# Optimization experiments

Hardware: AMD Instinct MI355X
Metric: run time of the kernel (lower is better)

The kernel has to match this reference:

```python
import jax, jax.numpy as jnp
import numpy as np

N = 100000
E = 3200000
D_IN = 512
D_HID = 128
D_OUT = 4


def setup_inputs() -> dict:
    key = jax.random.key(0)
    k1, k2, k3, k4, k5, k6 = jax.random.split(key, 6)
    x = jax.random.normal(k1, (N, D_IN), dtype=jnp.float32)
    edge_index = jax.random.randint(k2, (2, E), 0, N, dtype=jnp.int64)
    # GCNConv params (Glorot-ish scale)
    W1 = jax.random.normal(k3, (D_IN, D_HID), dtype=jnp.float32) / np.sqrt(D_IN)
    b1 = jax.random.normal(k4, (D_HID,), dtype=jnp.float32) * 0.01
    W2 = jax.random.normal(k5, (D_HID, D_OUT), dtype=jnp.float32) / np.sqrt(D_HID)
    b2 = jax.random.normal(k6, (D_OUT,), dtype=jnp.float32) * 0.01
    return {"x": x, "edge_index": edge_index, "W1": W1, "b1": b1, "W2": W2, "b2": b2}


def _gcn_conv(x, W, b, src, dst, deg_inv_sqrt):
    # h = X W, then symmetric-normalized aggregation with self-loops (PyG GCNConv default)
    h = x @ W                                   # [N, F_out]
    norm = deg_inv_sqrt[src] * deg_inv_sqrt[dst]  # [E]
    agg = jax.ops.segment_sum(h[src] * norm[:, None], dst, num_segments=x.shape[0])
    # self-loop contribution: norm_ii = deg_inv_sqrt[i]^2
    agg = agg + h * (deg_inv_sqrt ** 2)[:, None]
    return agg + b


def reference(x, edge_index, W1, b1, W2, b2):
    src, dst = edge_index[0], edge_index[1]
    # degree with added self-loops (edge weights = 1)
    deg = jax.ops.segment_sum(jnp.ones((E,), dtype=x.dtype), dst, num_segments=N) + 1.0
    deg_inv_sqrt = jax.lax.rsqrt(deg)
    h = jax.nn.relu(_gcn_conv(x, W1, b1, src, dst, deg_inv_sqrt))
    out = _gcn_conv(h, W2, b2, src, dst, deg_inv_sqrt)
    return out
```

## Files before the change

kernel.cpp:

```cpp
#include <hip/hip_runtime.h>
#include <hip/hip_fp16.h>

#define DIN 512
#define DHID 128
#define DOUT 4
#define BSH 8
#define PA_CHUNK 8192

typedef _Float16 f16x8 __attribute__((ext_vector_type(8)));
typedef _Float16 f16x4 __attribute__((ext_vector_type(4)));
typedef float    f32x4 __attribute__((ext_vector_type(4)));

#define GLOAD_LDS(gp, lp)                                                     \
  __builtin_amdgcn_global_load_lds(                                           \
      (const __attribute__((address_space(1))) void*)(gp),                    \
      (__attribute__((address_space(3))) void*)(lp), 16, 0, 0)

__global__ void detect_i64_k(const int* __restrict__ raw, int* __restrict__ flag) {
  if (blockIdx.x == 0 && threadIdx.x == 0) {
    int z = 1;
    for (int k = 0; k < 8; ++k)
      if (raw[2 * k + 1] != 0) z = 0;
    flag[0] = z;
  }
}

__global__ __launch_bounds__(256) void bcount_k(const int* __restrict__ raw,
                                                const int* __restrict__ flag,
                                                int* __restrict__ gbcnt, int E) {
  __shared__ int h[512];
  const int tid = threadIdx.x;
  const int f = flag[0];
  for (int i = tid; i < 512; i += 256) h[i] = 0;
  __syncthreads();
  const size_t e0 = (size_t)blockIdx.x * PA_CHUNK;
  #pragma unroll
  for (int k = 0; k < 32; ++k) {
    size_t e = e0 + (size_t)k * 256 + tid;
    if (e < (size_t)E) {
      int d = f ? raw[2 * ((size_t)E + e)] : raw[(size_t)E + e];
      atomicAdd(&h[d >> BSH], 1);
    }
  }
  __syncthreads();
  for (int i = tid; i < 512; i += 256)
    if (h[i]) atomicAdd(&gbcnt[i], h[i]);
}

__global__ __launch_bounds__(512) void bscan_k(const int* __restrict__ gbcnt,
                                               int* __restrict__ boffs,
                                               int* __restrict__ bcur,
                                               int* __restrict__ offs,
                                               int nbkt, int N, int E) {
  __shared__ int sm[512];
  int t = threadIdx.x;
  int v = (t < nbkt) ? gbcnt[t] : 0;
  int x = v;
  sm[t] = x;
  __syncthreads();
  #pragma unroll
  for (int o = 1; o < 512; o <<= 1) {
    int y = (t >= o) ? sm[t - o] : 0;
    __syncthreads();
    x += y;
    sm[t] = x;
    __syncthreads();
  }
  if (t < nbkt) {
    boffs[t] = x - v;
    bcur[t] = x - v;
  }
  if (t == 0) {
    boffs[nbkt] = E;
    offs[N] = E;
  }
}

__global__ __launch_bounds__(256) void binA_k(const int* __restrict__ raw,
                                              const int* __restrict__ flag,
                                              int* __restrict__ bcur,
                                              unsigned* __restrict__ pairs, int E) {
  __shared__ int hist[512];
  __shared__ int base[512];
  const int tid = threadIdx.x;
  const int f = flag[0];
  const size_t e0 = (size_t)blockIdx.x * PA_CHUNK;
  for (int i = tid; i < 512; i += 256) hist[i] = 0;
  __syncthreads();
  int es[32], ed[32];
  #pragma unroll
  for (int k = 0; k < 32; ++k) {
    size_t e = e0 + (size_t)k * 256 + tid;
    if (e < (size_t)E) {
      es[k] = f ? raw[2 * e] : raw[e];
      ed[k] = f ? raw[2 * ((size_t)E + e)] : raw[(size_t)E + e];
      atomicAdd(&hist[ed[k] >> BSH], 1);
    } else {
      ed[k] = -1;
    }
  }
  __syncthreads();
  for (int i = tid; i < 512; i += 256) {
    int c = hist[i];
    base[i] = c ? atomicAdd(&bcur[i], c) : 0;
    hist[i] = 0;
  }
  __syncthreads();
  #pragma unroll
  for (int k = 0; k < 32; ++k) {
    if (ed[k] >= 0) {
      int b = ed[k] >> BSH;
      int pos = base[b] + atomicAdd(&hist[b], 1);
      pairs[pos] = ((unsigned)es[k] << 8) | ((unsigned)ed[k] & 255u);
    }
  }
}

__global__ __launch_bounds__(256) void binB_k(const unsigned* __restrict__ pairs,
                                              const int* __restrict__ boffs,
                                              int* __restrict__ csr,
                                              int* __restrict__ offs,
                                              float* __restrict__ dis, int N) {
  __shared__ int lcnt[256];
  __shared__ int sc[256];
  const int tid = threadIdx.x;
  const int n0 = blockIdx.x << BSH;
  const int lo = boffs[blockIdx.x];
  const int hi = boffs[blockIdx.x + 1];
  lcnt[tid] = 0;
  __syncthreads();
  for (int j = lo + tid; j < hi; j += 256) atomicAdd(&lcnt[(int)(pairs[j] & 255u)], 1);
  __syncthreads();
  int v = lcnt[tid];
  int x = v;
  sc[tid] = x;
  __syncthreads();
  #pragma unroll
  for (int o = 1; o < 256; o <<= 1) {
    int y = (tid >= o) ? sc[tid - o] : 0;
    __syncthreads();
    x += y;
    sc[tid] = x;
    __syncthreads();
  }
  const int base = lo + x - v;
  const int node = n0 + tid;
  if (node < N) {
    offs[node] = base;
    dis[node] = rsqrtf((float)v + 1.0f);
  }
  __syncthreads();
  lcnt[tid] = base;
  __syncthreads();
  for (int j = lo + tid; j < hi; j += 256) {
    unsigned p = pairs[j];
    int dl = (int)(p & 255u);
    int pos = atomicAdd(&lcnt[dl], 1);
    csr[pos] = (int)(p >> 8);
  }
}

__global__ __launch_bounds__(256) void wsplit_k(const float* __restrict__ W1,
                                                __half* __restrict__ Bt2) {
  int idx = blockIdx.x * 256 + threadIdx.x;
  if (idx >= DIN * DHID) return;
  int k = idx >> 7;
  int n = idx & 127;
  int kt = k >> 5, kk = k & 31;
  float w = W1[idx];
  _Float16 hi = (_Float16)w;
  _Float16 lo = (_Float16)(w - (float)hi);
  size_t base = (size_t)(kt * 128 + n) * 64;
  Bt2[base + kk]      = *(__half*)&hi;
  Bt2[base + 32 + kk] = *(__half*)&lo;
}

__global__ __launch_bounds__(256, 2) void gemm1_k(const float* __restrict__ A,
                                                  const __half* __restrict__ Bt2,
                                                  const float* __restrict__ dis,
                                                  __half* __restrict__ hs, int N) {
  __shared__ char smem[49152];
  char* const sB = smem + 32768;
  const int tid = threadIdx.x;
  const int wave = tid >> 6, lane = tid & 63;
  const int lr = lane & 15, quad = lane >> 4;
  const int m0 = blockIdx.x * 128;
  const int mbase = (wave >> 1) * 64;
  const int nbase = (wave & 1) * 64;
  const int wbase = (tid & ~63) * 16;

  f32x4 acc[4][4];
  #pragma unroll
  for (int mt = 0; mt < 4; ++mt)
    #pragma unroll
    for (int nt = 0; nt < 4; ++nt) acc[mt][nt] = (f32x4){0.f, 0.f, 0.f, 0.f};

  const float*  agp[4];
  const __half* bgp[4];
  #pragma unroll
  for (int l = 0; l < 4; ++l) {
    int d16 = l * 256 + tid;
    int row = d16 >> 3;
    int chk = (d16 & 7) ^ (row & 7);
    int gr = m0 + row;
    if (gr >= N) gr = N - 1;
    agp[l] = A + (size_t)gr * DIN + chk * 4;
    bgp[l] = Bt2 + (size_t)row * 64 + chk * 8;
  }

  #pragma unroll
  for (int l = 0; l < 4; ++l)
    GLOAD_LDS(agp[l], smem + l * 4096 + wbase);
  #pragma unroll
  for (int l = 0; l < 4; ++l)
    GLOAD_LDS(bgp[l], sB + l * 4096 + wbase);

  int cur = 0;
  for (int kt = 0; kt < 16; ++kt) {
    if (kt < 15) {
      char* dA = smem + (cur ^ 1) * 16384;
      #pragma unroll
      for (int l = 0; l < 4; ++l)
        GLOAD_LDS(agp[l] + (kt + 1) * 32, dA + l * 4096 + wbase);
      asm volatile("s_waitcnt vmcnt(4)" ::: "memory");
    } else {
      asm volatile("s_waitcnt vmcnt(0)" ::: "memory");
    }
    __builtin_amdgcn_s_barrier();
    asm volatile("" ::: "memory");
    char* sA = smem + cur * 16384;
    f16x8 ah[4], al[4];
    #pragma unroll
    for (int mt = 0; mt < 4; ++mt) {
      int r = mbase + mt * 16 + lr;
      f32x4 v0 = *(const f32x4*)(sA + r * 128 + (((2 * quad + 0) ^ (r & 7)) << 4));
      f32x4 v1 = *(const f32x4*)(sA + r * 128 + (((2 * quad + 1) ^ (r & 7)) << 4));
      _Float16 c0 = (_Float16)v0[0], c1 = (_Float16)v0[1],
               c2 = (_Float16)v0[2], c3 = (_Float16)v0[3],
               c4 = (_Float16)v1[0], c5 = (_Float16)v1[1],
               c6 = (_Float16)v1[2], c7 = (_Float16)v1[3];
      ah[mt] = (f16x8){c0, c1, c2, c3, c4, c5, c6, c7};
      al[mt] = (f16x8){(_Float16)(v0[0] - (float)c0), (_Float16)(v0[1] - (float)c1),
                       (_Float16)(v0[2] - (float)c2), (_Float16)(v0[3] - (float)c3),
                       (_Float16)(v1[0] - (float)c4), (_Float16)(v1[1] - (float)c5),
                       (_Float16)(v1[2] - (float)c6), (_Float16)(v1[3] - (float)c7)};
    }
    #pragma unroll
    for (int nt = 0; nt < 4; ++nt) {
      int c = nbase + nt * 16 + lr;
      f16x8 bh = *(const f16x8*)(sB + c * 128 + (((0 + quad) ^ (c & 7)) << 4));
      f16x8 bl = *(const f16x8*)(sB + c * 128 + (((4 + quad) ^ (c & 7)) << 4));
      #pragma unroll
      for (int mt = 0; mt < 4; ++mt)
        acc[mt][nt] = __builtin_amdgcn_mfma_f32_16x16x32_f16(al[mt], bh, acc[mt][nt], 0, 0, 0);
      #pragma unroll
      for (int mt = 0; mt < 4; ++mt)
        acc[mt][nt] = __builtin_amdgcn_mfma_f32_16x16x32_f16(ah[mt], bl, acc[mt][nt], 0, 0, 0);
      #pragma unroll
      for (int mt = 0; mt < 4; ++mt)
        acc[mt][nt] = __builtin_amdgcn_mfma_f32_16x16x32_f16(ah[mt], bh, acc[mt][nt], 0, 0, 0);
    }
    __builtin_amdgcn_sched_barrier(0);
    __builtin_amdgcn_s_barrier();
    asm volatile("" ::: "memory");
    if (kt < 15) {
      #pragma unroll
      for (int l = 0; l < 4; ++l)
        GLOAD_LDS(bgp[l] + (size_t)(kt + 1) * 8192, sB + l * 4096 + wbase);
    }
    cur ^= 1;
  }
  _Float16* sep = (_Float16*)smem;
  #pragma unroll
  for (int mt = 0; mt < 4; ++mt) {
    #pragma unroll
    for (int r = 0; r < 4; ++r) {
      int row = mbase + mt * 16 + quad * 4 + r;
      int gr = m0 + row;
      float dv = dis[gr < N ? gr : (N - 1)];
      #pragma unroll
      for (int nt = 0; nt < 4; ++nt) {
        int col = nbase + nt * 16 + lr;
        sep[row * 136 + col] = (_Float16)(acc[mt][nt][r] * dv);
      }
    }
  }
  __syncthreads();
  #pragma unroll
  for (int l = 0; l < 8; ++l) {
    int idx = l * 256 + tid;
    int row = idx >> 4;
    int c = (idx & 15) << 3;
    int gr = m0 + row;
    if (gr < N)
      *(uint4*)(hs + (size_t)gr * DHID + c) = *(uint4*)&sep[row * 136 + c];
  }
}

__global__ __launch_bounds__(256) void agg1_k(const __half* __restrict__ hs,
                                              const float* __restrict__ dis,
                                              const int* __restrict__ offs,
                                              const int* __restrict__ csr,
                                              const float* __restrict__ W2,
                                              const float* __restrict__ b1,
                                              float* __restrict__ gs, int N) {
  const int wid = threadIdx.x >> 6;
  const int lane = threadIdx.x & 63;
  const int i = blockIdx.x * 4 + wid;
  if (i >= N) return;
  const int f = lane * 2;
  const __half* hp = hs + f;
  float ax = 0.f, ay = 0.f;
  const int beg = offs[i], end = offs[i + 1];
  for (int base = beg; base < end; base += 64) {
    int sj = 0;
    if (base + lane < end) sj = csr[base + lane];
    const int n = min(64, end - base);
    int t = 0;
    for (; t + 8 <= n; t += 8) {
      int s0 = __shfl(sj, t + 0, 64), s1 = __shfl(sj, t + 1, 64);
      int s2 = __shfl(sj, t + 2, 64), s3 = __shfl(sj, t + 3, 64);
      int s4 = __shfl(sj, t + 4, 64), s5 = __shfl(sj, t + 5, 64);
      int s6 = __shfl(sj, t + 6, 64), s7 = __shfl(sj, t + 7, 64);
      __half2 h0 = *(const __half2*)(hp + (size_t)s0 * DHID);
      __half2 h1 = *(const __half2*)(hp + (size_t)s1 * DHID);
      __half2 h2 = *(const __half2*)(hp + (size_t)s2 * DHID);
      __half2 h3 = *(const __half2*)(hp + (size_t)s3 * DHID);
      __half2 h4 = *(const __half2*)(hp + (size_t)s4 * DHID);
      __half2 h5 = *(const __half2*)(hp + (size_t)s5 * DHID);
      __half2 h6 = *(const __half2*)(hp + (size_t)s6 * DHID);
      __half2 h7 = *(const __half2*)(hp + (size_t)s7 * DHID);
      float2 f0 = __half22float2(h0), f1 = __half22float2(h1);
      float2 f2 = __half22float2(h2), f3 = __half22float2(h3);
      float2 f4 = __half22float2(h4), f5 = __half22float2(h5);
      float2 f6 = __half22float2(h6), f7 = __half22float2(h7);
      ax += ((f0.x + f1.x) + (f2.x + f3.x)) + ((f4.x + f5.x) + (f6.x + f7.x));
      ay += ((f0.y + f1.y) + (f2.y + f3.y)) + ((f4.y + f5.y) + (f6.y + f7.y));
    }
    for (; t < n; ++t) {
      int s = __shfl(sj, t, 64);
      float2 hf = __half22float2(*(const __half2*)(hp + (size_t)s * DHID));
      ax += hf.x;
      ay += hf.y;
    }
  }
  {
    float2 hf = __half22float2(*(const __half2*)(hp + (size_t)i * DHID));
    ax += hf.x;
    ay += hf.y;
  }
  const float di = dis[i];
  float v0 = fmaxf(fmaf(ax, di, b1[f]), 0.f);
  float v1 = fmaxf(fmaf(ay, di, b1[f + 1]), 0.f);
  float p0 = fmaf(v0, W2[f * 4 + 0], v1 * W2[f * 4 + 4]);
  float p1 = fmaf(v0, W2[f * 4 + 1], v1 * W2[f * 4 + 5]);
  float p2 = fmaf(v0, W2[f * 4 + 2], v1 * W2[f * 4 + 6]);
  float p3 = fmaf(v0, W2[f * 4 + 3], v1 * W2[f * 4 + 7]);
  #pragma unroll
  for (int o = 32; o > 0; o >>= 1) {
    p0 += __shfl_xor(p0, o, 64);
    p1 += __shfl_xor(p1, o, 64);
    p2 += __shfl_xor(p2, o, 64);
    p3 += __shfl_xor(p3, o, 64);
  }
  if (lane == 0)
    *(float4*)(gs + (size_t)i * DOUT) = make_float4(p0 * di, p1 * di, p2 * di, p3 * di);
}

__global__ __launch_bounds__(256) void agg2_k(const float* __restrict__ gs,
                                              const float* __restrict__ dis,
                                              const int* __restrict__ offs,
                                              const int* __restrict__ csr,
                                              const float* __restrict__ b2,
                                              float* __restrict__ out, int N) {
  int i = blockIdx.x * 256 + threadIdx.x;
  if (i >= N) return;
  float a0 = 0.f, a1 = 0.f, a2 = 0.f, a3 = 0.f;
  const int beg = offs[i], end = offs[i + 1];
  int j = beg;
  for (; j + 4 <= end; j += 4) {
    int s0 = csr[j], s1 = csr[j + 1], s2 = csr[j + 2], s3 = csr[j + 3];
    float4 g0 = *(const float4*)(gs + (size_t)s0 * DOUT);
    float4 g1 = *(const float4*)(gs + (size_t)s1 * DOUT);
    float4 g2 = *(const float4*)(gs + (size_t)s2 * DOUT);
    float4 g3 = *(const float4*)(gs + (size_t)s3 * DOUT);
    a0 += (g0.x + g1.x) + (g2.x + g3.x);
    a1 += (g0.y + g1.y) + (g2.y + g3.y);
    a2 += (g0.z + g1.z) + (g2.z + g3.z);
    a3 += (g0.w + g1.w) + (g2.w + g3.w);
  }
  for (; j < end; ++j) {
    int s = csr[j];
    float4 gv = *(const float4*)(gs + (size_t)s * DOUT);
    a0 += gv.x; a1 += gv.y; a2 += gv.z; a3 += gv.w;
  }
  const float di = dis[i];
  float4 gi = *(const float4*)(gs + (size_t)i * DOUT);
  float4 o4;
  o4.x = fmaf(a0 + gi.x, di, b2[0]);
  o4.y = fmaf(a1 + gi.y, di, b2[1]);
  o4.z = fmaf(a2 + gi.z, di, b2[2]);
  o4.w = fmaf(a3 + gi.w, di, b2[3]);
  *(float4*)(out + (size_t)i * DOUT) = o4;
}

extern "C" void kernel_launch(void* const* d_in, const int* in_sizes, int n_in,
                              void* d_out, int out_size, void* d_ws, size_t ws_size,
                              hipStream_t stream) {
  const float* x  = (const float*)d_in[0];
  const int*   raw = (const int*)d_in[1];
  const float* W1 = (const float*)d_in[2];
  const float* b1 = (const float*)d_in[3];
  const float* W2 = (const float*)d_in[4];
  const float* b2 = (const float*)d_in[5];
  float* out = (float*)d_out;

  const int N = in_sizes[0] / DIN;
  const int E = in_sizes[1] / 2;

  char* ws = (char*)d_ws;
  size_t off = 0;
  auto carve = [&](size_t bytes) -> char* {
    char* p = ws + off;
    off = (off + bytes + 255) & ~(size_t)255;
    return p;
  };
  float*    dis  = (float*)carve((size_t)N * 4);
  int*      offs = (int*)carve((size_t)(N + 1) * 4);
  int*      csr  = (int*)carve((size_t)E * 4);
  unsigned* pairs= (unsigned*)carve((size_t)E * 4);
  int*      boffs= (int*)carve(513 * 4);
  int*      bcur = (int*)carve(512 * 4);
  int*      gbcnt= (int*)carve(512 * 4);
  int*      flag = (int*)carve(256);
  __half*   Bt2  = (__half*)carve((size_t)DIN * DHID * 2 * 2);
  __half*   hs   = (__half*)carve((size_t)N * DHID * 2);
  float*    gs   = (float*)carve((size_t)N * DOUT * 4);
  (void)ws_size; (void)n_in; (void)out_size;

  const int gN = (N + 255) / 256;
  const int nbkt = (N + (1 << BSH) - 1) >> BSH;
  const int gA = (E + PA_CHUNK - 1) / PA_CHUNK;

  detect_i64_k<<<1, 64, 0, stream>>>(raw, flag);
  hipMemsetAsync(gbcnt, 0, 512 * 4, stream);
  bcount_k<<<gA, 256, 0, stream>>>(raw, flag, gbcnt, E);
  bscan_k<<<1, 512, 0, stream>>>(gbcnt, boffs, bcur, offs, nbkt, N, E);
  binA_k<<<gA, 256, 0, stream>>>(raw, flag, bcur, pairs, E);
  binB_k<<<nbkt, 256, 0, stream>>>(pairs, boffs, csr, offs, dis, N);
  wsplit_k<<<(DIN * DHID + 255) / 256, 256, 0, stream>>>(W1, Bt2);
  gemm1_k<<<(N + 127) / 128, 256, 0, stream>>>(x, Bt2, dis, hs, N);
  agg1_k<<<(N + 3) / 4, 256, 0, stream>>>(hs, dis, offs, csr, W2, b1, gs, N);
  agg2_k<<<gN, 256, 0, stream>>>(gs, dis, offs, csr, b2, out, N);
}
```

Baseline: 533.1 us.

## Fuse preprocessing kernels and split agg1 wave into two half-wave edge streams

The dtype-detect, bucket-count and W1-split kernels are merged into one launch, and each block recomputes the int64 flag locally instead of reading it from a separate kernel's output. This removes two launches and a serial dependency. agg1 now lets each half-wave handle alternate edges with 8-byte loads of 4 features per lane, then combines the halves with a cross-half shuffle. The goal is more gathers in flight per wave and fewer load instructions, at the cost of an extra reduction step and slightly more registers.

```diff
diff --git a/kernel.cpp b/kernel.cpp
--- a/kernel.cpp
+++ b/kernel.cpp
@@ -16,23 +16,37 @@
       (const __attribute__((address_space(1))) void*)(gp),                    \
       (__attribute__((address_space(3))) void*)(lp), 16, 0, 0)
 
-__global__ void detect_i64_k(const int* __restrict__ raw, int* __restrict__ flag) {
-  if (blockIdx.x == 0 && threadIdx.x == 0) {
+__global__ __launch_bounds__(256) void pre_k(const int* __restrict__ raw,
+                                             const float* __restrict__ W1,
+                                             int* __restrict__ gbcnt,
+                                             __half* __restrict__ Bt2,
+                                             int E, int gA) {
+  if (blockIdx.x >= gA) {
+    int idx = (blockIdx.x - gA) * 256 + threadIdx.x;
+    if (idx >= DIN * DHID) return;
+    int k = idx >> 7;
+    int n = idx & 127;
+    int kt = k >> 5, kk = k & 31;
+    float w = W1[idx];
+    _Float16 hi = (_Float16)w;
+    _Float16 lo = (_Float16)(w - (float)hi);
+    size_t base = (size_t)(kt * 128 + n) * 64;
+    Bt2[base + kk]      = *(__half*)&hi;
+    Bt2[base + 32 + kk] = *(__half*)&lo;
+    return;
+  }
+  __shared__ int h[512];
+  __shared__ int sflag;
+  const int tid = threadIdx.x;
+  if (tid == 0) {
     int z = 1;
     for (int k = 0; k < 8; ++k)
       if (raw[2 * k + 1] != 0) z = 0;
-    flag[0] = z;
-  }
-}
-
-__global__ __launch_bounds__(256) void bcount_k(const int* __restrict__ raw,
-                                                const int* __restrict__ flag,
-                                                int* __restrict__ gbcnt, int E) {
-  __shared__ int h[512];
-  const int tid = threadIdx.x;
-  const int f = flag[0];
+    sflag = z;
+  }
   for (int i = tid; i < 512; i += 256) h[i] = 0;
   __syncthreads();
+  const int f = sflag;
   const size_t e0 = (size_t)blockIdx.x * PA_CHUNK;
   #pragma unroll
   for (int k = 0; k < 32; ++k) {
@@ -77,16 +91,22 @@
 }
 
 __global__ __launch_bounds__(256) void binA_k(const int* __restrict__ raw,
-                                              const int* __restrict__ flag,
                                               int* __restrict__ bcur,
                                               unsigned* __restrict__ pairs, int E) {
   __shared__ int hist[512];
   __shared__ int base[512];
+  __shared__ int sflag;
   const int tid = threadIdx.x;
-  const int f = flag[0];
+  if (tid == 0) {
+    int z = 1;
+    for (int k = 0; k < 8; ++k)
+      if (raw[2 * k + 1] != 0) z = 0;
+    sflag = z;
+  }
+  for (int i = tid; i < 512; i += 256) hist[i] = 0;
+  __syncthreads();
+  const int f = sflag;
   const size_t e0 = (size_t)blockIdx.x * PA_CHUNK;
-  for (int i = tid; i < 512; i += 256) hist[i] = 0;
-  __syncthreads();
   int es[32], ed[32];
   #pragma unroll
   for (int k = 0; k < 32; ++k) {
@@ -158,21 +178,6 @@
     int pos = atomicAdd(&lcnt[dl], 1);
     csr[pos] = (int)(p >> 8);
   }
-}
-
-__global__ __launch_bounds__(256) void wsplit_k(const float* __restrict__ W1,
-                                                __half* __restrict__ Bt2) {
-  int idx = blockIdx.x * 256 + threadIdx.x;
-  if (idx >= DIN * DHID) return;
-  int k = idx >> 7;
-  int n = idx & 127;
-  int kt = k >> 5, kk = k & 31;
-  float w = W1[idx];
-  _Float16 hi = (_Float16)w;
-  _Float16 lo = (_Float16)(w - (float)hi);
-  size_t base = (size_t)(kt * 128 + n) * 64;
-  Bt2[base + kk]      = *(__half*)&hi;
-  Bt2[base + 32 + kk] = *(__half*)&lo;
 }
 
 __global__ __launch_bounds__(256, 2) void gemm1_k(const float* __restrict__ A,
@@ -308,56 +313,81 @@
   const int lane = threadIdx.x & 63;
   const int i = blockIdx.x * 4 + wid;
   if (i >= N) return;
-  const int f = lane * 2;
-  const __half* hp = hs + f;
-  float ax = 0.f, ay = 0.f;
+  const int half = lane >> 5;
+  const int li = lane & 31;
+  const __half* hp = hs + li * 4;
+  float a0 = 0.f, a1 = 0.f, a2 = 0.f, a3 = 0.f;
   const int beg = offs[i], end = offs[i + 1];
   for (int base = beg; base < end; base += 64) {
     int sj = 0;
     if (base + lane < end) sj = csr[base + lane];
     const int n = min(64, end - base);
     int t = 0;
-    for (; t + 8 <= n; t += 8) {
-      int s0 = __shfl(sj, t + 0, 64), s1 = __shfl(sj, t + 1, 64);
-      int s2 = __shfl(sj, t + 2, 64), s3 = __shfl(sj, t + 3, 64);
-      int s4 = __shfl(sj, t + 4, 64), s5 = __shfl(sj, t + 5, 64);
-      int s6 = __shfl(sj, t + 6, 64), s7 = __shfl(sj, t + 7, 64);
-      __half2 h0 = *(const __half2*)(hp + (size_t)s0 * DHID);
-      __half2 h1 = *(const __half2*)(hp + (size_t)s1 * DHID);
-      __half2 h2 = *(const __half2*)(hp + (size_t)s2 * DHID);
-      __half2 h3 = *(const __half2*)(hp + (size_t)s3 * DHID);
-      __half2 h4 = *(const __half2*)(hp + (size_t)s4 * DHID);
-      __half2 h5 = *(const __half2*)(hp + (size_t)s5 * DHID);
-      __half2 h6 = *(const __half2*)(hp + (size_t)s6 * DHID);
-      __half2 h7 = *(const __half2*)(hp + (size_t)s7 * DHID);
-      float2 f0 = __half22float2(h0), f1 = __half22float2(h1);
-      float2 f2 = __half22float2(h2), f3 = __half22float2(h3);
-      float2 f4 = __half22float2(h4), f5 = __half22float2(h5);
-      float2 f6 = __half22float2(h6), f7 = __half22float2(h7);
-      ax += ((f0.x + f1.x) + (f2.x + f3.x)) + ((f4.x + f5.x) + (f6.x + f7.x));
-      ay += ((f0.y + f1.y) + (f2.y + f3.y)) + ((f4.y + f5.y) + (f6.y + f7.y));
-    }
-    for (; t < n; ++t) {
-      int s = __shfl(sj, t, 64);
-      float2 hf = __half22float2(*(const __half2*)(hp + (size_t)s * DHID));
-      ax += hf.x;
-      ay += hf.y;
-    }
-  }
+    for (; t + 16 <= n; t += 16) {
+      int s0 = __shfl(sj, t + 0  + half, 64);
+      int s1 = __shfl(sj, t + 2  + half, 64);
+      int s2 = __shfl(sj, t + 4  + half, 64);
+      int s3 = __shfl(sj, t + 6  + half, 64);
+      int s4 = __shfl(sj, t + 8  + half, 64);
+      int s5 = __shfl(sj, t + 10 + half, 64);
+      int s6 = __shfl(sj, t + 12 + half, 64);
+      int s7 = __shfl(sj, t + 14 + half, 64);
+      short4 h0 = *(const short4*)(hp + (size_t)s0 * DHID);
+      short4 h1 = *(const short4*)(hp + (size_t)s1 * DHID);
+      short4 h2 = *(const short4*)(hp + (size_t)s2 * DHID);
+      short4 h3 = *(const short4*)(hp + (size_t)s3 * DHID);
+      short4 h4 = *(const short4*)(hp + (size_t)s4 * DHID);
+      short4 h5 = *(const short4*)(hp + (size_t)s5 * DHID);
+      short4 h6 = *(const short4*)(hp + (size_t)s6 * DHID);
+      short4 h7 = *(const short4*)(hp + (size_t)s7 * DHID);
+      #define ACC4(hv)                                                         \
+      {                                                                        \
+        float2 fa = __half22float2(*(const __half2*)&(hv).x);                  \
+        float2 fb = __half22float2(*(const __half2*)&(hv).z);                  \
+        a0 += fa.x; a1 += fa.y; a2 += fb.x; a3 += fb.y;                        \
+      }
+      ACC4(h0) ACC4(h1) ACC4(h2) ACC4(h3)
+      ACC4(h4) ACC4(h5) ACC4(h6) ACC4(h7)
+      #undef ACC4
+    }
+    for (; t < n; t += 2) {
+      int e = t + half;
+      bool ok = e < n;
+      int s = __shfl(sj, ok ? e : 0, 64);
+      if (ok) {
+        short4 hv = *(const short4*)(hp + (size_t)s * DHID);
+        float2 fa = __half22float2(*(const __half2*)&hv.x);
+        float2 fb = __half22float2(*(const __half2*)&hv.z);
+        a0 += fa.x; a1 += fa.y; a2 += fb.x; a3 += fb.y;
+      }
+    }
+  }
+  a0 += __shfl_xor(a0, 32, 64);
+  a1 += __shfl_xor(a1, 32, 64);
+  a2 += __shfl_xor(a2, 32, 64);
+  a3 += __shfl_xor(a3, 32, 64);
   {
-    float2 hf = __half22float2(*(const __half2*)(hp + (size_t)i * DHID));
-    ax += hf.x;
-    ay += hf.y;
+    short4 hv = *(const short4*)(hp + (size_t)i * DHID);
+    float2 fa = __half22float2(*(const __half2*)&hv.x);
+    float2 fb = __half22float2(*(const __half2*)&hv.z);
+    a0 += fa.x; a1 += fa.y; a2 += fb.x; a3 += fb.y;
   }
   const float di = dis[i];
-  float v0 = fmaxf(fmaf(ax, di, b1[f]), 0.f);
-  float v1 = fmaxf(fmaf(ay, di, b1[f + 1]), 0.f);
-  float p0 = fmaf(v0, W2[f * 4 + 0], v1 * W2[f * 4 + 4]);
-  float p1 = fmaf(v0, W2[f * 4 + 1], v1 * W2[f * 4 + 5]);
-  float p2 = fmaf(v0, W2[f * 4 + 2], v1 * W2[f * 4 + 6]);
-  float p3 = fmaf(v0, W2[f * 4 + 3], v1 * W2[f * 4 + 7]);
-  #pragma unroll
-  for (int o = 32; o > 0; o >>= 1) {
+  float4 bv = *(const float4*)(b1 + li * 4);
+  float v0 = fmaxf(fmaf(a0, di, bv.x), 0.f);
+  float v1 = fmaxf(fmaf(a1, di, bv.y), 0.f);
+  float v2 = fmaxf(fmaf(a2, di, bv.z), 0.f);
+  float v3 = fmaxf(fmaf(a3, di, bv.w), 0.f);
+  float4 w0 = *(const float4*)(W2 + (size_t)(li * 4 + 0) * 4);
+  float4 w1 = *(const float4*)(W2 + (size_t)(li * 4 + 1) * 4);
+  float4 w2 = *(const float4*)(W2 + (size_t)(li * 4 + 2) * 4);
+  float4 w3 = *(const float4*)(W2 + (size_t)(li * 4 + 3) * 4);
+  float p0 = fmaf(v0, w0.x, fmaf(v1, w1.x, fmaf(v2, w2.x, v3 * w3.x)));
+  float p1 = fmaf(v0, w0.y, fmaf(v1, w1.y, fmaf(v2, w2.y, v3 * w3.y)));
+  float p2 = fmaf(v0, w0.z, fmaf(v1, w1.z, fmaf(v2, w2.z, v3 * w3.z)));
+  float p3 = fmaf(v0, w0.w, fmaf(v1, w1.w, fmaf(v2, w2.w, v3 * w3.w)));
+  #pragma unroll
+  for (int o = 16; o > 0; o >>= 1) {
     p0 += __shfl_xor(p0, o, 64);
     p1 += __shfl_xor(p1, o, 64);
     p2 += __shfl_xor(p2, o, 64);
@@ -432,7 +462,6 @@
   int*      boffs= (int*)carve(513 * 4);
   int*      bcur = (int*)carve(512 * 4);
   int*      gbcnt= (int*)carve(512 * 4);
-  int*      flag = (int*)carve(256);
   __half*   Bt2  = (__half*)carve((size_t)DIN * DHID * 2 * 2);
   __half*   hs   = (__half*)carve((size_t)N * DHID * 2);
   float*    gs   = (float*)carve((size_t)N * DOUT * 4);
@@ -441,14 +470,13 @@
   const int gN = (N + 255) / 256;
   const int nbkt = (N + (1 << BSH) - 1) >> BSH;
   const int gA = (E + PA_CHUNK - 1) / PA_CHUNK;
-
-  detect_i64_k<<<1, 64, 0, stream>>>(raw, flag);
+  const int gW = (DIN * DHID + 255) / 256;
+
   hipMemsetAsync(gbcnt, 0, 512 * 4, stream);
-  bcount_k<<<gA, 256, 0, stream>>>(raw, flag, gbcnt, E);
+  pre_k<<<gA + gW, 256, 0, stream>>>(raw, W1, gbcnt, Bt2, E, gA);
   bscan_k<<<1, 512, 0, stream>>>(gbcnt, boffs, bcur, offs, nbkt, N, E);
-  binA_k<<<gA, 256, 0, stream>>>(raw, flag, bcur, pairs, E);
+  binA_k<<<gA, 256, 0, stream>>>(raw, bcur, pairs, E);
   binB_k<<<nbkt, 256, 0, stream>>>(pairs, boffs, csr, offs, dis, N);
-  wsplit_k<<<(DIN * DHID + 255) / 256, 256, 0, stream>>>(W1, Bt2);
   gemm1_k<<<(N + 127) / 128, 256, 0, stream>>>(x, Bt2, dis, hs, N);
   agg1_k<<<(N + 3) / 4, 256, 0, stream>>>(hs, dis, offs, csr, W2, b1, gs, N);
   agg2_k<<<gN, 256, 0, stream>>>(gs, dis, offs, csr, b2, out, N);
```

Result: no change. 529.9 us (-0.6%).
